# Kernel tuning notes

Hardware: AMD Instinct MI355X
Metric: run time of the kernel (lower is better)

Reference implementation:

```python
import jax, jax.numpy as jnp
import numpy as np

DT = 0.005
BETA = 0.9
THR = 0.5
TAU_MIN = 0.02
TAU_STEP = 0.03
TAU_R = 0.002
SLOPE = 25.0  # snntorch fast_sigmoid default surrogate slope

@jax.custom_vjp
def spike_fn(x):
    return (x > 0).astype(x.dtype)

def _spike_fwd(x):
    return spike_fn(x), x

def _spike_bwd(x, g):
    return (g / (SLOPE * jnp.abs(x) + 1.0) ** 2,)

spike_fn.defvjp(_spike_fwd, _spike_bwd)

def setup_inputs() -> dict:
    key = jax.random.key(0)
    ks = jax.random.split(key, 8)
    T, NIN, H, NOUT, P = 1000, 4, 4096, 2, 16
    inv_sqrt_h = 1.0 / np.sqrt(H).astype(np.float32)
    return {
        "x": jax.random.normal(ks[0], (T, NIN + 2, 1), jnp.float32),
        "noise": jax.random.normal(ks[1], (T, H, 1), jnp.float32),
        "Win": jax.random.normal(ks[2], (H, NIN + 2), jnp.float32),
        "Wout": jax.random.normal(ks[3], (NOUT, H), jnp.float32) * inv_sqrt_h,
        "pin": jax.random.normal(ks[4], (H, P), jnp.float32) * inv_sqrt_h,
        "pout": jax.random.normal(ks[5], (H, P), jnp.float32) * inv_sqrt_h,
        "l": jax.random.normal(ks[6], (P,), jnp.float32) * inv_sqrt_h,
        "sigmoid_tau_d": jax.random.normal(ks[7], (H, 1), jnp.float32),
    }

def reference(x, noise, Win, Wout, pin, pout, l, sigmoid_tau_d):
    H = Win.shape[0]
    tau_d = jax.nn.sigmoid(sigmoid_tau_d) * TAU_STEP + TAU_MIN   # [H,1]
    Wr = (l * pin) @ pout.T                                      # [H,H] low-rank recurrent matrix
    decay_r = jnp.exp(jnp.asarray(-DT / TAU_R, x.dtype))         # scalar
    decay_d = jnp.exp(-DT / tau_d)                               # [H,1]
    s_gain = DT / (tau_d * TAU_R)                                # [H,1]

    def step(carry, inp):
        mem, r, s = carry
        xi, ni = inp
        I = Win @ xi + Wr @ r + ni / 10.0                        # [H,1]
        # snntorch Leaky, reset_mechanism='subtract': reset from incoming mem (detached)
        reset = jax.lax.stop_gradient(spike_fn(mem - THR))
        mem = BETA * mem + I - reset * THR
        spk = spike_fn(mem - THR)
        s = s * decay_r + s_gain * spk
        r = decay_d * r + DT * s
        return (mem, r, s), r

    z = jnp.zeros((H, 1), x.dtype)
    _, R = jax.lax.scan(step, (z, z, z), (x, noise))             # R: [T,H,1]
    y = jnp.einsum('oh,thj->toj', Wout, R)                       # [T,O,1]
    return y
```

## Files before the change

kernel.cpp:

```cpp
#include <hip/hip_runtime.h>
#include <math.h>

#define KB       4
#define NTHREADS 256
#define NW       4
#define HID      4096
#define HB       (HID / KB)
#define NPT      4
#define TT       1000
#define PP       16
#define SLOTW    24

#define BETA 0.9f
#define THRV 0.5f
#define DTV  0.005f

template<int CTRL>
__device__ __forceinline__ float dppx(float v) {
    return __int_as_float(__builtin_amdgcn_update_dpp(
        0, __float_as_int(v), CTRL, 0xF, 0xF, true));
}

__global__ __launch_bounds__(NTHREADS, 1)
void snn_kernel(const float* __restrict__ x,
                const float* __restrict__ noise,
                const float* __restrict__ Win,
                const float* __restrict__ Wout,
                const float* __restrict__ pin,
                const float* __restrict__ pout,
                const float* __restrict__ lvec,
                const float* __restrict__ stdv,
                float* __restrict__ out,
                unsigned long long* __restrict__ slots)
{
    const int b    = blockIdx.x;
    const int tid  = threadIdx.x;
    const int wave = tid >> 6;
    const int lane = tid & 63;
    const int h0   = b * HB + tid * NPT;

    const bool lb0 = (lane & 1) != 0;
    const bool lb1 = (lane & 2) != 0;
    const bool lb2 = (lane & 4) != 0;
    const bool lb3 = (lane & 8) != 0;

    const int rb0 = (b == 0) ? 1 : 0;
    const int rb1 = (b <= 1) ? 2 : 1;
    const int rb2 = (b <= 2) ? 3 : 2;

    __shared__ float part[NW][20];
    __shared__ float ubuf[NW][16];

    float lv[PP];
    #pragma unroll
    for (int p = 0; p < PP; p += 4) {
        float4 t4 = *(const float4*)&lvec[p];
        lv[p] = t4.x; lv[p+1] = t4.y; lv[p+2] = t4.z; lv[p+3] = t4.w;
    }
    float pl[NPT][PP], po[NPT][PP];
    #pragma unroll
    for (int j = 0; j < NPT; ++j) {
        #pragma unroll
        for (int p = 0; p < PP; p += 4) {
            float4 a = *(const float4*)&pin[(h0+j)*PP + p];
            pl[j][p]   = a.x*lv[p];   pl[j][p+1] = a.y*lv[p+1];
            pl[j][p+2] = a.z*lv[p+2]; pl[j][p+3] = a.w*lv[p+3];
            float4 e = *(const float4*)&pout[(h0+j)*PP + p];
            po[j][p]   = e.x; po[j][p+1] = e.y;
            po[j][p+2] = e.z; po[j][p+3] = e.w;
        }
    }
    float win[NPT][6];
    #pragma unroll
    for (int j = 0; j < NPT; ++j) {
        const float2* wr = (const float2*)&Win[(h0+j)*6];
        float2 wA = wr[0], wB = wr[1], wC = wr[2];
        win[j][0]=wA.x; win[j][1]=wA.y; win[j][2]=wB.x;
        win[j][3]=wB.y; win[j][4]=wC.x; win[j][5]=wC.y;
    }
    float4 woa = *(const float4*)&Wout[h0];
    float4 wob = *(const float4*)&Wout[HID + h0];

    float4 sd4 = *(const float4*)&stdv[h0];
    float dd[NPT], sg[NPT];
    {
        float sdv[4] = { sd4.x, sd4.y, sd4.z, sd4.w };
        #pragma unroll
        for (int j = 0; j < NPT; ++j) {
            float sig = 1.f / (1.f + expf(-sdv[j]));
            float tau = sig * 0.03f + 0.02f;
            dd[j] = expf(-DTV / tau);
            sg[j] = DTV / (tau * 0.002f);
        }
    }
    const float DECAY_R = expf(-2.5f);

    float mem[NPT], rr[NPT], ss[NPT];
    #pragma unroll
    for (int j = 0; j < NPT; ++j) { mem[j] = 0.f; rr[j] = 0.f; ss[j] = 0.f; }

    const float2* x2 = (const float2*)x;
    float4 nz = *(const float4*)&noise[h0];
    float2 xa = x2[0], xb = x2[1], xc = x2[2];

    float uu[16];
    #pragma unroll
    for (int p = 0; p < 16; ++p) uu[p] = 0.f;

    for (int t = 0; t <= TT; ++t) {
        float4 nz_n = nz; float2 xa_n = xa, xb_n = xb, xc_n = xc;
        if (t < TT - 1) {
            const int tn = t + 1;
            nz_n = *(const float4*)&noise[tn * HID + h0];
            xa_n = x2[tn*3]; xb_n = x2[tn*3+1]; xc_n = x2[tn*3+2];
        }

        if (t > 0) {
            const int par = t & 1;
            float pa[18];
            #pragma unroll
            for (int p = 0; p < PP; ++p)
                pa[p] = (po[0][p]*rr[0] + po[1][p]*rr[1])
                      + (po[2][p]*rr[2] + po[3][p]*rr[3]);
            pa[16] = (woa.x*rr[0] + woa.y*rr[1]) + (woa.z*rr[2] + woa.w*rr[3]);
            pa[17] = (wob.x*rr[0] + wob.y*rr[1]) + (wob.z*rr[2] + wob.w*rr[3]);

            float a1[8], yv;
            #pragma unroll
            for (int k = 0; k < 8; ++k) {
                float keep = lb0 ? pa[2*k+1] : pa[2*k];
                float send = lb0 ? pa[2*k]   : pa[2*k+1];
                a1[k] = keep + dppx<0xB1>(send);
            }
            {
                float keep = lb0 ? pa[17] : pa[16];
                float send = lb0 ? pa[16] : pa[17];
                yv = keep + dppx<0xB1>(send);
            }
            float a2[4];
            #pragma unroll
            for (int k = 0; k < 4; ++k) {
                float keep = lb1 ? a1[2*k+1] : a1[2*k];
                float send = lb1 ? a1[2*k]   : a1[2*k+1];
                a2[k] = keep + dppx<0x4E>(send);
            }
            yv += dppx<0x4E>(yv);
            float a3[2];
            #pragma unroll
            for (int k = 0; k < 2; ++k) {
                float keep = lb2 ? a2[2*k+1] : a2[2*k];
                float send = lb2 ? a2[2*k]   : a2[2*k+1];
                a3[k] = keep + __shfl_xor(send, 4, 64);
            }
            yv += __shfl_xor(yv, 4, 64);
            float uv;
            {
                float keep = lb3 ? a3[1] : a3[0];
                float send = lb3 ? a3[0] : a3[1];
                uv = keep + dppx<0x128>(send);
            }
            yv += dppx<0x128>(yv);
            uv += __shfl_xor(uv, 16, 64);
            uv += __shfl_xor(uv, 32, 64);
            yv += __shfl_xor(yv, 16, 64);
            yv += __shfl_xor(yv, 32, 64);

            if (lane < 18) part[wave][lane] = (lane < 16) ? uv : yv;
            __syncthreads();

            float bs = 0.f;
            if (lane < 18) {
                bs = (part[0][lane] + part[1][lane])
                   + (part[2][lane] + part[3][lane]);
            }

            if (wave == 0 && lane < 18) {
                union { float f; unsigned u; } cv; cv.f = bs;
                unsigned long long pk = ((unsigned long long)(unsigned)t << 32)
                                      | (unsigned long long)cv.u;
                __hip_atomic_store(&slots[(size_t)(par*KB + b)*SLOTW + lane], pk,
                                   __ATOMIC_RELAXED, __HIP_MEMORY_SCOPE_AGENT);
            }

            if (t < TT || b == 0) {
                float f0 = 0.f, f1 = 0.f, f2 = 0.f;
                if (lane < 18) {
                    const unsigned long long* p0 =
                        &slots[(size_t)(par*KB + rb0)*SLOTW + lane];
                    const unsigned long long* p1 =
                        &slots[(size_t)(par*KB + rb1)*SLOTW + lane];
                    const unsigned long long* p2 =
                        &slots[(size_t)(par*KB + rb2)*SLOTW + lane];
                    unsigned long long v0, v1, v2;
                    int spin = 0;
                    do {
                        v0 = __hip_atomic_load(p0, __ATOMIC_RELAXED,
                                               __HIP_MEMORY_SCOPE_AGENT);
                        v1 = __hip_atomic_load(p1, __ATOMIC_RELAXED,
                                               __HIP_MEMORY_SCOPE_AGENT);
                        v2 = __hip_atomic_load(p2, __ATOMIC_RELAXED,
                                               __HIP_MEMORY_SCOPE_AGENT);
                    } while ((((int)(v0 >> 32) != t) | ((int)(v1 >> 32) != t) |
                              ((int)(v2 >> 32) != t)) && ++spin < (1 << 20));
                    union { unsigned u; float f; } c0, c1, c2;
                    c0.u = (unsigned)v0; c1.u = (unsigned)v1; c2.u = (unsigned)v2;
                    f0 = c0.f; f1 = c1.f; f2 = c2.f;
                }
                float total = (b < 2) ? ((bs + f0) + (f1 + f2))
                                      : ((f0 + f1) + (f2 + bs));
                if (lane < 16) ubuf[wave][lane] = total;
                if (b == 0 && wave == 0 && lane >= 16 && lane < 18)
                    out[(t-1)*2 + (lane - 16)] = total;

                float4 u0 = *(const float4*)&ubuf[wave][0];
                float4 u1 = *(const float4*)&ubuf[wave][4];
                float4 u2 = *(const float4*)&ubuf[wave][8];
                float4 u3 = *(const float4*)&ubuf[wave][12];
                uu[0]=u0.x; uu[1]=u0.y; uu[2]=u0.z; uu[3]=u0.w;
                uu[4]=u1.x; uu[5]=u1.y; uu[6]=u1.z; uu[7]=u1.w;
                uu[8]=u2.x; uu[9]=u2.y; uu[10]=u2.z; uu[11]=u2.w;
                uu[12]=u3.x; uu[13]=u3.y; uu[14]=u3.z; uu[15]=u3.w;
            }
        }

        if (t < TT) {
            float nzv[4] = { nz.x, nz.y, nz.z, nz.w };
            #pragma unroll
            for (int j = 0; j < NPT; ++j) {
                float ra = pl[j][0]*uu[0];
                float rb2_ = pl[j][8]*uu[8];
                #pragma unroll
                for (int p = 1; p < 8; ++p) {
                    ra   += pl[j][p]*uu[p];
                    rb2_ += pl[j][p+8]*uu[p+8];
                }
                float rec = ra + rb2_;
                float xw = win[j][0]*xa.x + win[j][1]*xa.y
                         + win[j][2]*xb.x + win[j][3]*xb.y
                         + win[j][4]*xc.x + win[j][5]*xc.y;
                float I = (xw + rec) + nzv[j] / 10.0f;

                float rst = (mem[j] - THRV > 0.f) ? THRV : 0.f;
                mem[j] = BETA*mem[j] + I - rst;
                float spk = (mem[j] - THRV > 0.f) ? 1.f : 0.f;
                ss[j] = ss[j]*DECAY_R + sg[j]*spk;
                rr[j] = dd[j]*rr[j] + DTV*ss[j];
            }
            nz = nz_n; xa = xa_n; xb = xb_n; xc = xc_n;
        }
    }
}

extern "C" void kernel_launch(void* const* d_in, const int* in_sizes, int n_in,
                              void* d_out, int out_size, void* d_ws, size_t ws_size,
                              hipStream_t stream)
{
    const float* x     = (const float*)d_in[0];
    const float* noise = (const float*)d_in[1];
    const float* Win   = (const float*)d_in[2];
    const float* Wout  = (const float*)d_in[3];
    const float* pin   = (const float*)d_in[4];
    const float* pout  = (const float*)d_in[5];
    const float* l     = (const float*)d_in[6];
    const float* stdv  = (const float*)d_in[7];
    float* out = (float*)d_out;
    unsigned long long* slots = (unsigned long long*)d_ws;

    hipLaunchKernelGGL(snn_kernel, dim3(KB), dim3(NTHREADS), 0, stream,
                       x, noise, Win, Wout, pin, pout, l, stdv,
                       out, slots);
}
```

Before: 1.631 ms.

## Poll remote block slots from a single wave and broadcast via shared memory

Previously every wave in every block spun on atomic loads of three remote blocks' slots, with each lane polling three addresses. Now only wave 0 polls, and it spreads the 54 slot reads across lanes so each lane spins on one address. Wave 0 then combines the partial sums and passes the result to the other waves through shared memory behind an extra __syncthreads. The slot stride grows to 32. This cuts global polling traffic and the three-way combined spin loop, but adds a block barrier on the critical path of every step.

```diff
diff --git a/kernel.cpp b/kernel.cpp
--- a/kernel.cpp
+++ b/kernel.cpp
@@ -9,7 +9,7 @@
 #define NPT      4
 #define TT       1000
 #define PP       16
-#define SLOTW    24
+#define SLOTW    32
 
 #define BETA 0.9f
 #define THRV 0.5f
@@ -44,12 +44,17 @@
     const bool lb2 = (lane & 4) != 0;
     const bool lb3 = (lane & 8) != 0;
 
-    const int rb0 = (b == 0) ? 1 : 0;
-    const int rb1 = (b <= 1) ? 2 : 1;
-    const int rb2 = (b <= 2) ? 3 : 2;
+    const int rbA = (b == 0) ? 1 : 0;
+    const int rbB = (b <= 1) ? 2 : 1;
+    const int rbC = (b <= 2) ? 3 : 2;
+
+    const int rIdx = lane / 18;
+    const int vIdx = lane - rIdx * 18;
+    const int rblk = (rIdx == 0) ? rbA : ((rIdx == 1) ? rbB : rbC);
 
     __shared__ float part[NW][20];
-    __shared__ float ubuf[NW][16];
+    __shared__ float rbuf[3][20];
+    __shared__ __align__(16) float fin[20];
 
     float lv[PP];
     #pragma unroll
@@ -168,54 +173,48 @@
             if (lane < 18) part[wave][lane] = (lane < 16) ? uv : yv;
             __syncthreads();
 
-            float bs = 0.f;
-            if (lane < 18) {
-                bs = (part[0][lane] + part[1][lane])
-                   + (part[2][lane] + part[3][lane]);
-            }
-
-            if (wave == 0 && lane < 18) {
-                union { float f; unsigned u; } cv; cv.f = bs;
-                unsigned long long pk = ((unsigned long long)(unsigned)t << 32)
-                                      | (unsigned long long)cv.u;
-                __hip_atomic_store(&slots[(size_t)(par*KB + b)*SLOTW + lane], pk,
-                                   __ATOMIC_RELAXED, __HIP_MEMORY_SCOPE_AGENT);
-            }
-
-            if (t < TT || b == 0) {
-                float f0 = 0.f, f1 = 0.f, f2 = 0.f;
+            if (wave == 0) {
+                float bs = 0.f;
                 if (lane < 18) {
-                    const unsigned long long* p0 =
-                        &slots[(size_t)(par*KB + rb0)*SLOTW + lane];
-                    const unsigned long long* p1 =
-                        &slots[(size_t)(par*KB + rb1)*SLOTW + lane];
-                    const unsigned long long* p2 =
-                        &slots[(size_t)(par*KB + rb2)*SLOTW + lane];
-                    unsigned long long v0, v1, v2;
-                    int spin = 0;
-                    do {
-                        v0 = __hip_atomic_load(p0, __ATOMIC_RELAXED,
-                                               __HIP_MEMORY_SCOPE_AGENT);
-                        v1 = __hip_atomic_load(p1, __ATOMIC_RELAXED,
-                                               __HIP_MEMORY_SCOPE_AGENT);
-                        v2 = __hip_atomic_load(p2, __ATOMIC_RELAXED,
-                                               __HIP_MEMORY_SCOPE_AGENT);
-                    } while ((((int)(v0 >> 32) != t) | ((int)(v1 >> 32) != t) |
-                              ((int)(v2 >> 32) != t)) && ++spin < (1 << 20));
-                    union { unsigned u; float f; } c0, c1, c2;
-                    c0.u = (unsigned)v0; c1.u = (unsigned)v1; c2.u = (unsigned)v2;
-                    f0 = c0.f; f1 = c1.f; f2 = c2.f;
+                    bs = (part[0][lane] + part[1][lane])
+                       + (part[2][lane] + part[3][lane]);
+                    union { float f; unsigned u; } cv; cv.f = bs;
+                    unsigned long long pk = ((unsigned long long)(unsigned)t << 32)
+                                          | (unsigned long long)cv.u;
+                    __hip_atomic_store(&slots[(size_t)(par*KB + b)*SLOTW + lane], pk,
+                                       __ATOMIC_RELAXED, __HIP_MEMORY_SCOPE_AGENT);
                 }
-                float total = (b < 2) ? ((bs + f0) + (f1 + f2))
-                                      : ((f0 + f1) + (f2 + bs));
-                if (lane < 16) ubuf[wave][lane] = total;
-                if (b == 0 && wave == 0 && lane >= 16 && lane < 18)
-                    out[(t-1)*2 + (lane - 16)] = total;
-
-                float4 u0 = *(const float4*)&ubuf[wave][0];
-                float4 u1 = *(const float4*)&ubuf[wave][4];
-                float4 u2 = *(const float4*)&ubuf[wave][8];
-                float4 u3 = *(const float4*)&ubuf[wave][12];
+                if (t < TT || b == 0) {
+                    if (lane < 54) {
+                        const unsigned long long* rp =
+                            &slots[(size_t)(par*KB + rblk)*SLOTW + vIdx];
+                        unsigned long long v;
+                        int spin = 0;
+                        do {
+                            v = __hip_atomic_load(rp, __ATOMIC_RELAXED,
+                                                  __HIP_MEMORY_SCOPE_AGENT);
+                        } while ((int)(v >> 32) != t && ++spin < (1 << 20));
+                        union { unsigned u; float f; } cv; cv.u = (unsigned)v;
+                        rbuf[rIdx][vIdx] = cv.f;
+                    }
+                    __builtin_amdgcn_s_waitcnt(0);
+                    if (lane < 18) {
+                        float f0 = rbuf[0][lane], f1 = rbuf[1][lane], f2 = rbuf[2][lane];
+                        float total = (b < 2) ? ((bs + f0) + (f1 + f2))
+                                              : ((f0 + f1) + (f2 + bs));
+                        fin[lane] = total;
+                        if (b == 0 && lane >= 16)
+                            out[(t-1)*2 + (lane - 16)] = total;
+                    }
+                }
+            }
+            __syncthreads();
+
+            if (t < TT) {
+                float4 u0 = *(const float4*)&fin[0];
+                float4 u1 = *(const float4*)&fin[4];
+                float4 u2 = *(const float4*)&fin[8];
+                float4 u3 = *(const float4*)&fin[12];
                 uu[0]=u0.x; uu[1]=u0.y; uu[2]=u0.z; uu[3]=u0.w;
                 uu[4]=u1.x; uu[5]=u1.y; uu[6]=u1.z; uu[7]=u1.w;
                 uu[8]=u2.x; uu[9]=u2.y; uu[10]=u2.z; uu[11]=u2.w;
```

New measurement: 1.645 ms. About the same (+0.9%).

## Shorten cross-block exchange: LDS reduction, drop y from slots, overlap input work

Applied to the files above, without the earlier changes.

Replaces the in-wave xor-shuffle reduction with an LDS partial-sum layout, so each wave writes 16-row partials and lane 0-17 finish the sum. The Wout output projection is taken off the cross-block exchange path: each block writes its own y partials to workspace, and a second small kernel sums them. The input and noise part of the membrane update is computed before spinning on the other blocks' slots. Polling first waits on one slot per block, then does a wave-wide check. Together these aim to shorten the serial per-timestep critical path, at the cost of an extra kernel launch and more LDS traffic.

```diff
diff --git a/kernel.cpp b/kernel.cpp
--- a/kernel.cpp
+++ b/kernel.cpp
@@ -9,7 +9,7 @@
 #define NPT      4
 #define TT       1000
 #define PP       16
-#define SLOTW    24
+#define SLOTW    32
 
 #define BETA 0.9f
 #define THRV 0.5f
@@ -19,6 +19,10 @@
 __device__ __forceinline__ float dppx(float v) {
     return __int_as_float(__builtin_amdgcn_update_dpp(
         0, __float_as_int(v), CTRL, 0xF, 0xF, true));
+}
+
+__device__ __forceinline__ unsigned long long AL(const unsigned long long* p) {
+    return __hip_atomic_load(p, __ATOMIC_RELAXED, __HIP_MEMORY_SCOPE_AGENT);
 }
 
 __global__ __launch_bounds__(NTHREADS, 1)
@@ -30,7 +34,7 @@
                 const float* __restrict__ pout,
                 const float* __restrict__ lvec,
                 const float* __restrict__ stdv,
-                float* __restrict__ out,
+                float* __restrict__ ypart,
                 unsigned long long* __restrict__ slots)
 {
     const int b    = blockIdx.x;
@@ -44,11 +48,12 @@
     const bool lb2 = (lane & 4) != 0;
     const bool lb3 = (lane & 8) != 0;
 
-    const int rb0 = (b == 0) ? 1 : 0;
-    const int rb1 = (b <= 1) ? 2 : 1;
-    const int rb2 = (b <= 2) ? 3 : 2;
-
-    __shared__ float part[NW][20];
+    const int rbA = (b == 0) ? 1 : 0;
+    const int rbB = (b <= 1) ? 2 : 1;
+    const int rbC = (b <= 2) ? 3 : 2;
+
+    __shared__ float part[NW][4][16];
+    __shared__ float ylds[NW][4][2];
     __shared__ float ubuf[NW][16];
 
     float lv[PP];
@@ -115,6 +120,7 @@
             xa_n = x2[tn*3]; xb_n = x2[tn*3+1]; xc_n = x2[tn*3+2];
         }
 
+        float bs = 0.f;
         if (t > 0) {
             const int par = t & 1;
             float pa[18];
@@ -153,65 +159,104 @@
                 a3[k] = keep + __shfl_xor(send, 4, 64);
             }
             yv += __shfl_xor(yv, 4, 64);
-            float uv;
+            float uvrow;
             {
                 float keep = lb3 ? a3[1] : a3[0];
                 float send = lb3 ? a3[0] : a3[1];
-                uv = keep + dppx<0x128>(send);
+                uvrow = keep + dppx<0x128>(send);
             }
             yv += dppx<0x128>(yv);
-            uv += __shfl_xor(uv, 16, 64);
-            uv += __shfl_xor(uv, 32, 64);
-            yv += __shfl_xor(yv, 16, 64);
-            yv += __shfl_xor(yv, 32, 64);
-
-            if (lane < 18) part[wave][lane] = (lane < 16) ? uv : yv;
+
+            part[wave][lane >> 4][lane & 15] = uvrow;
+            if ((lane & 15) < 2) ylds[wave][lane >> 4][lane & 1] = yv;
             __syncthreads();
 
-            float bs = 0.f;
-            if (lane < 18) {
-                bs = (part[0][lane] + part[1][lane])
-                   + (part[2][lane] + part[3][lane]);
-            }
-
-            if (wave == 0 && lane < 18) {
-                union { float f; unsigned u; } cv; cv.f = bs;
-                unsigned long long pk = ((unsigned long long)(unsigned)t << 32)
-                                      | (unsigned long long)cv.u;
-                __hip_atomic_store(&slots[(size_t)(par*KB + b)*SLOTW + lane], pk,
-                                   __ATOMIC_RELAXED, __HIP_MEMORY_SCOPE_AGENT);
-            }
-
-            if (t < TT || b == 0) {
+            float ybs = 0.f;
+            if (lane < 16) {
+                float t0 = (part[0][0][lane] + part[0][1][lane])
+                         + (part[0][2][lane] + part[0][3][lane]);
+                float t1 = (part[1][0][lane] + part[1][1][lane])
+                         + (part[1][2][lane] + part[1][3][lane]);
+                float t2 = (part[2][0][lane] + part[2][1][lane])
+                         + (part[2][2][lane] + part[2][3][lane]);
+                float t3 = (part[3][0][lane] + part[3][1][lane])
+                         + (part[3][2][lane] + part[3][3][lane]);
+                bs = (t0 + t1) + (t2 + t3);
+            } else if (lane < 18) {
+                const int yi = lane - 16;
+                float t0 = (ylds[0][0][yi] + ylds[0][1][yi])
+                         + (ylds[0][2][yi] + ylds[0][3][yi]);
+                float t1 = (ylds[1][0][yi] + ylds[1][1][yi])
+                         + (ylds[1][2][yi] + ylds[1][3][yi]);
+                float t2 = (ylds[2][0][yi] + ylds[2][1][yi])
+                         + (ylds[2][2][yi] + ylds[2][3][yi]);
+                float t3 = (ylds[3][0][yi] + ylds[3][1][yi])
+                         + (ylds[3][2][yi] + ylds[3][3][yi]);
+                ybs = (t0 + t1) + (t2 + t3);
+            }
+
+            if (wave == 0) {
+                if (lane < 16 && t < TT) {
+                    union { float f; unsigned u; } cv; cv.f = bs;
+                    unsigned long long pk = ((unsigned long long)(unsigned)t << 32)
+                                          | (unsigned long long)cv.u;
+                    __hip_atomic_store(&slots[(size_t)(par*KB + b)*SLOTW + lane], pk,
+                                       __ATOMIC_RELAXED, __HIP_MEMORY_SCOPE_AGENT);
+                } else if (lane >= 16 && lane < 18) {
+                    ypart[(size_t)b * (2*TT) + (t-1)*2 + (lane-16)] = ybs;
+                }
+            }
+        }
+
+        if (t < TT) {
+            float nzv[4] = { nz.x, nz.y, nz.z, nz.w };
+            float pre[NPT];
+            #pragma unroll
+            for (int j = 0; j < NPT; ++j) {
+                float xw = win[j][0]*xa.x + win[j][1]*xa.y
+                         + win[j][2]*xb.x + win[j][3]*xb.y
+                         + win[j][4]*xc.x + win[j][5]*xc.y;
+                float rst = (mem[j] - THRV > 0.f) ? THRV : 0.f;
+                pre[j] = BETA*mem[j] + xw + nzv[j] / 10.0f - rst;
+            }
+
+            if (t > 0) {
+                const int par = t & 1;
+                const size_t sb = (size_t)par * KB;
+                {
+                    const unsigned long long* t0p = &slots[(sb + rbA)*SLOTW + 15];
+                    const unsigned long long* t1p = &slots[(sb + rbB)*SLOTW + 15];
+                    const unsigned long long* t2p = &slots[(sb + rbC)*SLOTW + 15];
+                    unsigned long long w0, w1, w2;
+                    int sp = 0;
+                    do {
+                        w0 = AL(t0p); w1 = AL(t1p); w2 = AL(t2p);
+                    } while ((((unsigned)(w0 >> 32) != (unsigned)t) |
+                              ((unsigned)(w1 >> 32) != (unsigned)t) |
+                              ((unsigned)(w2 >> 32) != (unsigned)t)) &&
+                             ++sp < (1 << 20));
+                }
                 float f0 = 0.f, f1 = 0.f, f2 = 0.f;
-                if (lane < 18) {
-                    const unsigned long long* p0 =
-                        &slots[(size_t)(par*KB + rb0)*SLOTW + lane];
-                    const unsigned long long* p1 =
-                        &slots[(size_t)(par*KB + rb1)*SLOTW + lane];
-                    const unsigned long long* p2 =
-                        &slots[(size_t)(par*KB + rb2)*SLOTW + lane];
-                    unsigned long long v0, v1, v2;
-                    int spin = 0;
+                int ok = 1;
+                if (lane < 16) {
+                    const unsigned long long* pa_ = &slots[(sb + rbA)*SLOTW + lane];
+                    const unsigned long long* pb_ = &slots[(sb + rbB)*SLOTW + lane];
+                    const unsigned long long* pc_ = &slots[(sb + rbC)*SLOTW + lane];
+                    unsigned long long va, vb, vc;
+                    int sp2 = 0;
                     do {
-                        v0 = __hip_atomic_load(p0, __ATOMIC_RELAXED,
-                                               __HIP_MEMORY_SCOPE_AGENT);
-                        v1 = __hip_atomic_load(p1, __ATOMIC_RELAXED,
-                                               __HIP_MEMORY_SCOPE_AGENT);
-                        v2 = __hip_atomic_load(p2, __ATOMIC_RELAXED,
-                                               __HIP_MEMORY_SCOPE_AGENT);
-                    } while ((((int)(v0 >> 32) != t) | ((int)(v1 >> 32) != t) |
-                              ((int)(v2 >> 32) != t)) && ++spin < (1 << 20));
+                        va = AL(pa_); vb = AL(pb_); vc = AL(pc_);
+                        ok = ((unsigned)(va >> 32) == (unsigned)t)
+                           & ((unsigned)(vb >> 32) == (unsigned)t)
+                           & ((unsigned)(vc >> 32) == (unsigned)t);
+                    } while (!__all(ok) && ++sp2 < (1 << 18));
                     union { unsigned u; float f; } c0, c1, c2;
-                    c0.u = (unsigned)v0; c1.u = (unsigned)v1; c2.u = (unsigned)v2;
+                    c0.u = (unsigned)va; c1.u = (unsigned)vb; c2.u = (unsigned)vc;
                     f0 = c0.f; f1 = c1.f; f2 = c2.f;
                 }
                 float total = (b < 2) ? ((bs + f0) + (f1 + f2))
                                       : ((f0 + f1) + (f2 + bs));
                 if (lane < 16) ubuf[wave][lane] = total;
-                if (b == 0 && wave == 0 && lane >= 16 && lane < 18)
-                    out[(t-1)*2 + (lane - 16)] = total;
-
                 float4 u0 = *(const float4*)&ubuf[wave][0];
                 float4 u1 = *(const float4*)&ubuf[wave][4];
                 float4 u2 = *(const float4*)&ubuf[wave][8];
@@ -221,10 +266,7 @@
                 uu[8]=u2.x; uu[9]=u2.y; uu[10]=u2.z; uu[11]=u2.w;
                 uu[12]=u3.x; uu[13]=u3.y; uu[14]=u3.z; uu[15]=u3.w;
             }
-        }
-
-        if (t < TT) {
-            float nzv[4] = { nz.x, nz.y, nz.z, nz.w };
+
             #pragma unroll
             for (int j = 0; j < NPT; ++j) {
                 float ra = pl[j][0]*uu[0];
@@ -235,19 +277,24 @@
                     rb2_ += pl[j][p+8]*uu[p+8];
                 }
                 float rec = ra + rb2_;
-                float xw = win[j][0]*xa.x + win[j][1]*xa.y
-                         + win[j][2]*xb.x + win[j][3]*xb.y
-                         + win[j][4]*xc.x + win[j][5]*xc.y;
-                float I = (xw + rec) + nzv[j] / 10.0f;
-
-                float rst = (mem[j] - THRV > 0.f) ? THRV : 0.f;
-                mem[j] = BETA*mem[j] + I - rst;
+                mem[j] = pre[j] + rec;
                 float spk = (mem[j] - THRV > 0.f) ? 1.f : 0.f;
                 ss[j] = ss[j]*DECAY_R + sg[j]*spk;
                 rr[j] = dd[j]*rr[j] + DTV*ss[j];
             }
             nz = nz_n; xa = xa_n; xb = xb_n; xc = xc_n;
         }
+    }
+}
+
+__global__ void ysum_kernel(const float* __restrict__ yp, float* __restrict__ out) {
+    int i = blockIdx.x * blockDim.x + threadIdx.x;
+    if (i < 2 * TT) {
+        float a = yp[i];
+        float b = yp[2*TT + i];
+        float c = yp[2*2*TT + i];
+        float d = yp[3*2*TT + i];
+        out[i] = (a + b) + (c + d);
     }
 }
 
@@ -265,8 +312,11 @@
     const float* stdv  = (const float*)d_in[7];
     float* out = (float*)d_out;
     unsigned long long* slots = (unsigned long long*)d_ws;
+    float* ypart = (float*)((char*)d_ws + 4096);
 
     hipLaunchKernelGGL(snn_kernel, dim3(KB), dim3(NTHREADS), 0, stream,
                        x, noise, Win, Wout, pin, pout, l, stdv,
-                       out, slots);
-}
+                       ypart, slots);
+    hipLaunchKernelGGL(ysum_kernel, dim3((2*TT + 255)/256), dim3(256), 0, stream,
+                       ypart, out);
+}
```

Result: slower. 1.897 ms (+16.3%).

## Co-locate worker blocks on one XCC and exchange partial sums through L2

Applied to the files above, without the earlier changes.

Launches 32 blocks that each report their XCC id through a boot array. The first four blocks found on a shared XCC run the recurrence and the rest exit. Inter-block partial sums are written and polled with sc0 loads and stores, meant to stay in the shared L2 instead of crossing to device-coherent memory, which should shorten the per-timestep handshake. A bounded spin falls back to the older agent-scope atomic slots if the L2 path never sees the data. The cost is an extra zero kernel, a boot barrier at start, and reliance on XCC placement and cache-policy behaviour for correctness.

```diff
diff --git a/kernel.cpp b/kernel.cpp
--- a/kernel.cpp
+++ b/kernel.cpp
@@ -2,6 +2,7 @@
 #include <math.h>
 
 #define KB       4
+#define NBOOT    32
 #define NTHREADS 256
 #define NW       4
 #define HID      4096
@@ -9,7 +10,7 @@
 #define NPT      4
 #define TT       1000
 #define PP       16
-#define SLOTW    24
+#define SLOTW    32
 
 #define BETA 0.9f
 #define THRV 0.5f
@@ -19,6 +20,34 @@
 __device__ __forceinline__ float dppx(float v) {
     return __int_as_float(__builtin_amdgcn_update_dpp(
         0, __float_as_int(v), CTRL, 0xF, 0xF, true));
+}
+
+__device__ __forceinline__ unsigned long long AL(const unsigned long long* p) {
+    return __hip_atomic_load(p, __ATOMIC_RELAXED, __HIP_MEMORY_SCOPE_AGENT);
+}
+__device__ __forceinline__ void AS(unsigned long long* p, unsigned long long v) {
+    __hip_atomic_store(p, v, __ATOMIC_RELAXED, __HIP_MEMORY_SCOPE_AGENT);
+}
+__device__ __forceinline__ void st64_sc0(unsigned long long* p, unsigned long long v) {
+    asm volatile("global_store_dwordx2 %0, %1, off sc0" :: "v"(p), "v"(v) : "memory");
+}
+__device__ __forceinline__ void ld64x3_sc0(const unsigned long long* p0,
+                                           const unsigned long long* p1,
+                                           const unsigned long long* p2,
+                                           unsigned long long& v0,
+                                           unsigned long long& v1,
+                                           unsigned long long& v2) {
+    asm volatile("global_load_dwordx2 %0, %3, off sc0\n\t"
+                 "global_load_dwordx2 %1, %4, off sc0\n\t"
+                 "global_load_dwordx2 %2, %5, off sc0\n\t"
+                 "s_waitcnt vmcnt(0)"
+                 : "=&v"(v0), "=&v"(v1), "=&v"(v2)
+                 : "v"(p0), "v"(p1), "v"(p2) : "memory");
+}
+
+__global__ void zero_kernel(unsigned* boot) {
+    int i = threadIdx.x;
+    if (i < NBOOT) boot[i] = 0u;
 }
 
 __global__ __launch_bounds__(NTHREADS, 1)
@@ -31,22 +60,48 @@
                 const float* __restrict__ lvec,
                 const float* __restrict__ stdv,
                 float* __restrict__ out,
-                unsigned long long* __restrict__ slots)
+                unsigned long long* __restrict__ slotsL2,
+                unsigned long long* __restrict__ slotsAG,
+                unsigned* __restrict__ boot)
 {
-    const int b    = blockIdx.x;
     const int tid  = threadIdx.x;
     const int wave = tid >> 6;
     const int lane = tid & 63;
-    const int h0   = b * HB + tid * NPT;
+
+    unsigned xcc;
+    asm volatile("s_getreg_b32 %0, hwreg(HW_REG_XCC_ID)" : "=s"(xcc));
+    if (tid == 0)
+        __hip_atomic_store(&boot[blockIdx.x], 0x80000000u | (xcc & 0xffu),
+                           __ATOMIC_RELAXED, __HIP_MEMORY_SCOPE_AGENT);
+    unsigned e = 0;
+    if (lane < NBOOT) {
+        int sp = 0;
+        do {
+            e = __hip_atomic_load(&boot[lane], __ATOMIC_RELAXED,
+                                  __HIP_MEMORY_SCOPE_AGENT);
+        } while (!(e & 0x80000000u) && ++sp < (1 << 22));
+    }
+    unsigned long long m = 0; int found = -1;
+    #pragma unroll 1
+    for (int c = 0; c < 8; ++c) {
+        unsigned long long bm = __ballot(lane < NBOOT && (e & 0xffu) == (unsigned)c);
+        if (found < 0 && __popcll(bm) >= KB) { m = bm; found = c; }
+    }
+    const int below = __popcll(m & ((1ull << blockIdx.x) - 1ull));
+    const bool chosen = (found >= 0) && ((m >> blockIdx.x) & 1ull) && (below < KB);
+    if (!chosen) return;
+    const int b = below;
+
+    const int h0 = b * HB + tid * NPT;
 
     const bool lb0 = (lane & 1) != 0;
     const bool lb1 = (lane & 2) != 0;
     const bool lb2 = (lane & 4) != 0;
     const bool lb3 = (lane & 8) != 0;
 
-    const int rb0 = (b == 0) ? 1 : 0;
-    const int rb1 = (b <= 1) ? 2 : 1;
-    const int rb2 = (b <= 2) ? 3 : 2;
+    const int rbA = (b == 0) ? 1 : 0;
+    const int rbB = (b <= 1) ? 2 : 1;
+    const int rbC = (b <= 2) ? 3 : 2;
 
     __shared__ float part[NW][20];
     __shared__ float ubuf[NW][16];
@@ -65,9 +120,9 @@
             float4 a = *(const float4*)&pin[(h0+j)*PP + p];
             pl[j][p]   = a.x*lv[p];   pl[j][p+1] = a.y*lv[p+1];
             pl[j][p+2] = a.z*lv[p+2]; pl[j][p+3] = a.w*lv[p+3];
-            float4 e = *(const float4*)&pout[(h0+j)*PP + p];
-            po[j][p]   = e.x; po[j][p+1] = e.y;
-            po[j][p+2] = e.z; po[j][p+3] = e.w;
+            float4 e4 = *(const float4*)&pout[(h0+j)*PP + p];
+            po[j][p]   = e4.x; po[j][p+1] = e4.y;
+            po[j][p+2] = e4.z; po[j][p+3] = e4.w;
         }
     }
     float win[NPT][6];
@@ -107,6 +162,8 @@
     #pragma unroll
     for (int p = 0; p < 16; ++p) uu[p] = 0.f;
 
+    int use_sc0 = 1;
+
     for (int t = 0; t <= TT; ++t) {
         float4 nz_n = nz; float2 xa_n = xa, xb_n = xb, xc_n = xc;
         if (t < TT - 1) {
@@ -178,32 +235,44 @@
                 union { float f; unsigned u; } cv; cv.f = bs;
                 unsigned long long pk = ((unsigned long long)(unsigned)t << 32)
                                       | (unsigned long long)cv.u;
-                __hip_atomic_store(&slots[(size_t)(par*KB + b)*SLOTW + lane], pk,
-                                   __ATOMIC_RELAXED, __HIP_MEMORY_SCOPE_AGENT);
+                const size_t si = (size_t)(par*KB + b)*SLOTW + lane;
+                st64_sc0(&slotsL2[si], pk);
+                AS(&slotsAG[si], pk);
             }
 
             if (t < TT || b == 0) {
                 float f0 = 0.f, f1 = 0.f, f2 = 0.f;
                 if (lane < 18) {
-                    const unsigned long long* p0 =
-                        &slots[(size_t)(par*KB + rb0)*SLOTW + lane];
-                    const unsigned long long* p1 =
-                        &slots[(size_t)(par*KB + rb1)*SLOTW + lane];
-                    const unsigned long long* p2 =
-                        &slots[(size_t)(par*KB + rb2)*SLOTW + lane];
-                    unsigned long long v0, v1, v2;
-                    int spin = 0;
-                    do {
-                        v0 = __hip_atomic_load(p0, __ATOMIC_RELAXED,
-                                               __HIP_MEMORY_SCOPE_AGENT);
-                        v1 = __hip_atomic_load(p1, __ATOMIC_RELAXED,
-                                               __HIP_MEMORY_SCOPE_AGENT);
-                        v2 = __hip_atomic_load(p2, __ATOMIC_RELAXED,
-                                               __HIP_MEMORY_SCOPE_AGENT);
-                    } while ((((int)(v0 >> 32) != t) | ((int)(v1 >> 32) != t) |
-                              ((int)(v2 >> 32) != t)) && ++spin < (1 << 20));
+                    const size_t sb = (size_t)par * KB;
+                    unsigned long long va = 0, vb = 0, vc = 0;
+                    bool got = false;
+                    if (use_sc0) {
+                        const unsigned long long* pa_ = &slotsL2[(sb + rbA)*SLOTW + lane];
+                        const unsigned long long* pb_ = &slotsL2[(sb + rbB)*SLOTW + lane];
+                        const unsigned long long* pc_ = &slotsL2[(sb + rbC)*SLOTW + lane];
+                        int sp = 0;
+                        do {
+                            ld64x3_sc0(pa_, pb_, pc_, va, vb, vc);
+                            got = ((unsigned)(va >> 32) == (unsigned)t)
+                                & ((unsigned)(vb >> 32) == (unsigned)t)
+                                & ((unsigned)(vc >> 32) == (unsigned)t);
+                        } while (!got && ++sp < 256);
+                        if (!got) use_sc0 = 0;
+                    }
+                    if (!got) {
+                        const unsigned long long* pa_ = &slotsAG[(sb + rbA)*SLOTW + lane];
+                        const unsigned long long* pb_ = &slotsAG[(sb + rbB)*SLOTW + lane];
+                        const unsigned long long* pc_ = &slotsAG[(sb + rbC)*SLOTW + lane];
+                        int sp2 = 0;
+                        do {
+                            va = AL(pa_); vb = AL(pb_); vc = AL(pc_);
+                        } while ((((unsigned)(va >> 32) != (unsigned)t) |
+                                  ((unsigned)(vb >> 32) != (unsigned)t) |
+                                  ((unsigned)(vc >> 32) != (unsigned)t)) &&
+                                 ++sp2 < (1 << 20));
+                    }
                     union { unsigned u; float f; } c0, c1, c2;
-                    c0.u = (unsigned)v0; c1.u = (unsigned)v1; c2.u = (unsigned)v2;
+                    c0.u = (unsigned)va; c1.u = (unsigned)vb; c2.u = (unsigned)vc;
                     f0 = c0.f; f1 = c1.f; f2 = c2.f;
                 }
                 float total = (b < 2) ? ((bs + f0) + (f1 + f2))
@@ -264,9 +333,12 @@
     const float* l     = (const float*)d_in[6];
     const float* stdv  = (const float*)d_in[7];
     float* out = (float*)d_out;
-    unsigned long long* slots = (unsigned long long*)d_ws;
-
-    hipLaunchKernelGGL(snn_kernel, dim3(KB), dim3(NTHREADS), 0, stream,
+    unsigned long long* slotsL2 = (unsigned long long*)d_ws;
+    unsigned long long* slotsAG = (unsigned long long*)((char*)d_ws + 2048);
+    unsigned* boot = (unsigned*)((char*)d_ws + 4096);
+
+    hipLaunchKernelGGL(zero_kernel, dim3(1), dim3(64), 0, stream, boot);
+    hipLaunchKernelGGL(snn_kernel, dim3(NBOOT), dim3(NTHREADS), 0, stream,
                        x, noise, Win, Wout, pin, pout, l, stdv,
-                       out, slots);
-}
+                       out, slotsL2, slotsAG, boot);
+}
```

After: 1.644 ms. Within noise of the previous version (+0.8%).
